# Performance work log

Hardware: AMD Instinct MI355X
Metric: run time of the kernel (lower is better)

The kernel has to match this reference:

```python
import jax, jax.numpy as jnp
import numpy as np
from jax import lax

V, D, L, H, MAXLEN = 32000, 512, 6, 8, 1024
DH = D // H
DFF = 4 * D
B, T = 8, 1024


def _ln(x, g, b, eps=1e-5):
    m = jnp.mean(x, axis=-1, keepdims=True)
    v = jnp.var(x, axis=-1, keepdims=True)
    return (x - m) * lax.rsqrt(v + eps) * g + b


def setup_inputs() -> dict:
    key = jax.random.key(0)
    ks = jax.random.split(key, 16)
    s = 0.02
    inp = {
        "idx": jax.random.randint(ks[0], (B, T), 0, V, dtype=jnp.int32),
        "wte": jax.random.normal(ks[1], (V, D), jnp.float32) * s,   # tied with head
        "wpe": jax.random.normal(ks[2], (MAXLEN, D), jnp.float32) * s,
        # per-layer stacked params [L, ...]
        "ln1_g": jnp.ones((L, D), jnp.float32),
        "ln1_b": jnp.zeros((L, D), jnp.float32),
        "w_qkv": jax.random.normal(ks[3], (L, D, 3 * D), jnp.float32) * s,
        "b_qkv": jnp.zeros((L, 3 * D), jnp.float32),
        "w_ao": jax.random.normal(ks[4], (L, D, D), jnp.float32) * s,
        "b_ao": jnp.zeros((L, D), jnp.float32),
        "ln2_g": jnp.ones((L, D), jnp.float32),
        "ln2_b": jnp.zeros((L, D), jnp.float32),
        "w_fc": jax.random.normal(ks[5], (L, D, DFF), jnp.float32) * s,
        "b_fc": jnp.zeros((L, DFF), jnp.float32),
        "w_pr": jax.random.normal(ks[6], (L, DFF, D), jnp.float32) * s,
        "b_pr": jnp.zeros((L, D), jnp.float32),
        "lnf_g": jnp.ones((D,), jnp.float32),
        "lnf_b": jnp.zeros((D,), jnp.float32),
    }
    return inp


def reference(idx, wte, wpe, ln1_g, ln1_b, w_qkv, b_qkv, w_ao, b_ao,
              ln2_g, ln2_b, w_fc, b_fc, w_pr, b_pr, lnf_g, lnf_b):
    Bx, Tx = idx.shape
    x = wte[idx] + wpe[:Tx]                      # [B,T,D]
    causal = jnp.tril(jnp.ones((Tx, Tx), bool))  # [T,T]
    scale = 1.0 / np.sqrt(DH)

    def block(x, p):
        (g1, b1, wqkv, bqkv, wao, bao, g2, b2, wfc, bfc, wpr, bpr) = p
        h = _ln(x, g1, b1)
        qkv = h @ wqkv + bqkv                    # [B,T,3D]
        q, k, v = jnp.split(qkv, 3, axis=-1)
        q = q.reshape(Bx, Tx, H, DH)
        k = k.reshape(Bx, Tx, H, DH)
        v = v.reshape(Bx, Tx, H, DH)
        att = jnp.einsum('bqhd,bkhd->bhqk', q, k) * scale
        att = jnp.where(causal, att, -jnp.inf)
        att = jax.nn.softmax(att, axis=-1)
        y = jnp.einsum('bhqk,bkhd->bqhd', att, v).reshape(Bx, Tx, D)
        x = x + y @ wao + bao
        h = _ln(x, g2, b2)
        h = jax.nn.gelu(h @ wfc + bfc, approximate=False)
        x = x + h @ wpr + bpr
        return x, None

    params = (ln1_g, ln1_b, w_qkv, b_qkv, w_ao, b_ao,
              ln2_g, ln2_b, w_fc, b_fc, w_pr, b_pr)
    x, _ = lax.scan(block, x, params)
    x = _ln(x, lnf_g, lnf_b)
    logits = x @ wte.T                           # tied head, [B,T,V]
    return logits
```

## Files before the change

### kernel.cpp

```cpp
#include <hip/hip_runtime.h>
#include <hip/hip_bf16.h>
#include <math.h>

#define V_   32000
#define D_   512
#define L_   6
#define H_   8
#define DH_  64
#define DFF_ 2048
#define B_   8
#define T_   1024
#define BT_  (B_*T_)

typedef __attribute__((ext_vector_type(4))) float f32x4;
typedef __attribute__((ext_vector_type(8))) short short8;
using bf16_t = __hip_bfloat16;

__device__ __forceinline__ float b2f(unsigned short u) {
    union { unsigned int i; float f; } v; v.i = ((unsigned int)u) << 16; return v.f;
}
__device__ __forceinline__ unsigned short f2b(float f) {
    bf16_t h = __float2bfloat16(f);
    return *reinterpret_cast<unsigned short*>(&h);
}
__device__ __forceinline__ void gl16(const void* g, void* l) {
    __builtin_amdgcn_global_load_lds((const __attribute__((address_space(1))) void*)g,
                                     (__attribute__((address_space(3))) void*)l, 16, 0, 0);
}
__device__ __forceinline__ float gelu_exact(float v) {
    return 0.5f * v * (1.0f + erff(v * 0.70710678118654752f));
}

__global__ __launch_bounds__(128) void embed_kernel(
        const int* __restrict__ idx, const float* __restrict__ wte,
        const float* __restrict__ wpe, float* __restrict__ x) {
    int bt = blockIdx.x;
    int t  = bt & (T_ - 1);
    int tok = idx[bt];
    const float4* wr = (const float4*)(wte + (size_t)tok * D_);
    const float4* pr = (const float4*)(wpe + (size_t)t * D_);
    float4* xr = (float4*)(x + (size_t)bt * D_);
    int i = threadIdx.x;
    float4 a = wr[i], b = pr[i];
    xr[i] = make_float4(a.x + b.x, a.y + b.y, a.z + b.z, a.w + b.w);
}

__global__ __launch_bounds__(128) void ln_kernel(
        const float* __restrict__ x, const float* __restrict__ g,
        const float* __restrict__ b, bf16_t* __restrict__ out) {
    int bt = blockIdx.x;
    int i  = threadIdx.x;
    float4 v = ((const float4*)(x + (size_t)bt * D_))[i];
    float s  = v.x + v.y + v.z + v.w;
    float sq = v.x*v.x + v.y*v.y + v.z*v.z + v.w*v.w;
    #pragma unroll
    for (int o = 32; o > 0; o >>= 1) {
        s  += __shfl_down(s,  o);
        sq += __shfl_down(sq, o);
    }
    __shared__ float ss[2], ssq[2];
    if ((i & 63) == 0) { ss[i >> 6] = s; ssq[i >> 6] = sq; }
    __syncthreads();
    float mean = (ss[0] + ss[1]) * (1.0f / D_);
    float var  = (ssq[0] + ssq[1]) * (1.0f / D_) - mean * mean;
    float rstd = rsqrtf(var + 1e-5f);
    float4 gg = ((const float4*)g)[i];
    float4 bb = ((const float4*)b)[i];
    ushort4 o4;
    o4.x = f2b((v.x - mean) * rstd * gg.x + bb.x);
    o4.y = f2b((v.y - mean) * rstd * gg.y + bb.y);
    o4.z = f2b((v.z - mean) * rstd * gg.z + bb.z);
    o4.w = f2b((v.w - mean) * rstd * gg.w + bb.w);
    ((ushort4*)(out + (size_t)bt * D_))[i] = o4;
}

__global__ __launch_bounds__(256) void conv_kernel(
        const float* __restrict__ s, bf16_t* __restrict__ d, int n4) {
    int i = blockIdx.x * 256 + threadIdx.x;
    if (i >= n4) return;
    float4 f = ((const float4*)s)[i];
    ushort4 u = make_ushort4(f2b(f.x), f2b(f.y), f2b(f.z), f2b(f.w));
    ((ushort4*)d)[i] = u;
}

__global__ __launch_bounds__(256) void tconv_kernel(
        const float* __restrict__ src, bf16_t* __restrict__ dst, int K, int N) {
    size_t ls = (size_t)K * N;
    const float* s = src + blockIdx.z * ls;
    bf16_t* d = dst + blockIdx.z * ls;
    __shared__ float tile[32][33];
    int n0 = blockIdx.x * 32, k0 = blockIdx.y * 32;
    int c = threadIdx.x & 31, r8 = threadIdx.x >> 5;
    #pragma unroll
    for (int i = 0; i < 4; ++i) {
        int r = r8 + i * 8;
        tile[r][c] = s[(size_t)(k0 + r) * N + n0 + c];
    }
    __syncthreads();
    #pragma unroll
    for (int i = 0; i < 4; ++i) {
        int r = r8 + i * 8;
        d[(size_t)(n0 + r) * K + k0 + c] = __float2bfloat16(tile[c][r]);
    }
}

template<int ACT, bool OBF, bool RES, bool CONVB>
__global__ __launch_bounds__(256) void mm_kernel(
        const bf16_t* __restrict__ A,
        const bf16_t* __restrict__ Bt,
        const float*  __restrict__ Bf,
        const float*  __restrict__ bias,
        const float*  __restrict__ res,
        void* __restrict__ Cout,
        int M, int N, int K)
{
    __shared__ __align__(16) unsigned short As[128 * 64];
    __shared__ __align__(16) unsigned short Bs[128 * 64];
    const int nwg = gridDim.x;
    const int orig = blockIdx.x;
    const int q8 = nwg >> 3, r8 = nwg & 7;
    const int xcd = orig & 7, lin = orig >> 3;
    const int wg = (xcd < r8) ? xcd * (q8 + 1) + lin
                              : r8 * (q8 + 1) + (xcd - r8) * q8 + lin;
    const int gym = M >> 7;
    const int by = wg % gym;
    const int bx = wg / gym;

    const int t    = threadIdx.x;
    const int row0 = by * 128;
    const int col0 = bx * 128;
    const int lane = t & 63;
    const int wid  = t >> 6;
    const int wm   = (wid & 1) * 64;
    const int wn   = (wid >> 1) * 64;
    const int fr   = lane & 15;
    const int fq   = lane >> 4;

    f32x4 acc[4][4];
    #pragma unroll
    for (int m = 0; m < 4; ++m)
        #pragma unroll
        for (int n = 0; n < 4; ++n)
            acc[m][n] = (f32x4)(0.0f);

    const unsigned short* Ab  = (const unsigned short*)A;
    const unsigned short* Btb = (const unsigned short*)Bt;

    for (int k0 = 0; k0 < K; k0 += 64) {
        __syncthreads();
        #pragma unroll
        for (int i = 0; i < 4; ++i) {
            int c = t + i * 256;
            int row = c >> 3;
            int sl  = (c & 7) ^ (row & 7);
            gl16(Ab + (size_t)(row0 + row) * K + k0 + sl * 8, As + (size_t)c * 8);
        }
        if (!CONVB) {
            #pragma unroll
            for (int i = 0; i < 4; ++i) {
                int c = t + i * 256;
                int row = c >> 3;
                int sl  = (c & 7) ^ (row & 7);
                gl16(Btb + (size_t)(col0 + row) * K + k0 + sl * 8, Bs + (size_t)c * 8);
            }
        } else {
            #pragma unroll
            for (int i = 0; i < 4; ++i) {
                int c = t + i * 256;
                int row = c >> 3;
                int sl  = (c & 7) ^ (row & 7);
                const float* sp = Bf + (size_t)(col0 + row) * K + k0 + sl * 8;
                float4 f0 = ((const float4*)sp)[0];
                float4 f1 = ((const float4*)sp)[1];
                short8 pk;
                pk[0] = f2b(f0.x); pk[1] = f2b(f0.y); pk[2] = f2b(f0.z); pk[3] = f2b(f0.w);
                pk[4] = f2b(f1.x); pk[5] = f2b(f1.y); pk[6] = f2b(f1.z); pk[7] = f2b(f1.w);
                *(short8*)(Bs + (size_t)c * 8) = pk;
            }
        }
        __syncthreads();

        #pragma unroll
        for (int kk = 0; kk < 2; ++kk) {
            short8 av[4], bv[4];
            #pragma unroll
            for (int m = 0; m < 4; ++m) {
                int R = wm + m * 16 + fr;
                int sl = (kk * 4 + fq) ^ (fr & 7);
                av[m] = *(const short8*)(As + (size_t)R * 64 + sl * 8);
            }
            #pragma unroll
            for (int n = 0; n < 4; ++n) {
                int R = wn + n * 16 + fr;
                int sl = (kk * 4 + fq) ^ (fr & 7);
                bv[n] = *(const short8*)(Bs + (size_t)R * 64 + sl * 8);
            }
            #pragma unroll
            for (int m = 0; m < 4; ++m)
                #pragma unroll
                for (int n = 0; n < 4; ++n)
                    acc[m][n] = __builtin_amdgcn_mfma_f32_16x16x32_bf16(av[m], bv[n], acc[m][n], 0, 0, 0);
        }
    }

    #pragma unroll
    for (int n = 0; n < 4; ++n) {
        int col = col0 + wn + n * 16 + fr;
        float bb = bias ? bias[col] : 0.0f;
        #pragma unroll
        for (int m = 0; m < 4; ++m) {
            int rbase = row0 + wm + m * 16 + fq * 4;
            #pragma unroll
            for (int r = 0; r < 4; ++r) {
                float v = acc[m][n][r] + bb;
                if (ACT == 1) v = gelu_exact(v);
                size_t off = (size_t)(rbase + r) * N + col;
                if (RES) v += res[off];
                if (OBF) ((bf16_t*)Cout)[off] = __float2bfloat16(v);
                else     ((float*)Cout)[off]  = v;
            }
        }
    }
}

#define MM8_PHASE(MH, NH, HALF, SRCB, R0, DSTB)                               \
  {                                                                           \
    short8 af[2][4]; short8 bg[2][2];                                         \
    _Pragma("unroll")                                                         \
    for (int ks = 0; ks < 2; ++ks) {                                          \
      _Pragma("unroll")                                                       \
      for (int m = 0; m < 4; ++m) {                                           \
        int row = ((MH)*4 + m)*32 + wm*16 + fr;                               \
        int sl  = (ks*4 + fq) ^ (fr & 7);                                     \
        af[ks][m] = *(const short8*)(curA + (size_t)row*64 + (size_t)sl*8);   \
      }                                                                       \
      _Pragma("unroll")                                                       \
      for (int n = 0; n < 2; ++n) {                                           \
        int col = ((NH)*2 + n)*64 + wn*16 + fr;                               \
        int sl  = (ks*4 + fq) ^ (fr & 7);                                     \
        bg[ks][n] = *(const short8*)(curB + (size_t)col*64 + (size_t)sl*8);   \
      }                                                                       \
    }                                                                         \
    if (pf) {                                                                 \
      _Pragma("unroll")                                                       \
      for (int i = 0; i < 2; ++i) {                                           \
        int c = (HALF)*1024 + i*512 + t;                                      \
        int row = c >> 3, sl = (c & 7) ^ (row & 7);                           \
        gl16(SRCB + (size_t)((R0) + row)*K + k0n + sl*8,                      \
             DSTB + (size_t)c*8);                                             \
      }                                                                       \
      asm volatile("s_waitcnt vmcnt(2)" ::: "memory");                        \
    } else if ((MH) == 0 && (NH) == 0) {                                      \
      asm volatile("s_waitcnt vmcnt(0)" ::: "memory");                        \
    }                                                                         \
    asm volatile("s_barrier" ::: "memory");                                   \
    asm volatile("s_waitcnt lgkmcnt(0)" ::: "memory");                        \
    __builtin_amdgcn_sched_barrier(0);                                        \
    __builtin_amdgcn_s_setprio(1);                                            \
    _Pragma("unroll")                                                         \
    for (int ks = 0; ks < 2; ++ks)                                            \
      _Pragma("unroll")                                                       \
      for (int m = 0; m < 4; ++m)                                             \
        _Pragma("unroll")                                                     \
        for (int n = 0; n < 2; ++n)                                           \
          acc[(MH)*4+m][(NH)*2+n] = __builtin_amdgcn_mfma_f32_16x16x32_bf16(  \
              af[ks][m], bg[ks][n], acc[(MH)*4+m][(NH)*2+n], 0, 0, 0);        \
    __builtin_amdgcn_s_setprio(0);                                            \
    __builtin_amdgcn_sched_barrier(0);                                        \
    asm volatile("s_barrier" ::: "memory");                                   \
  }

template<int ACT, bool OBF>
__global__ __launch_bounds__(512) void mm8_kernel(
        const bf16_t* __restrict__ A,
        const bf16_t* __restrict__ Bt,
        const float*  __restrict__ bias,
        void* __restrict__ Cout,
        int M, int N, int K)
{
    __shared__ __align__(16) unsigned short sA[2][256 * 64];
    __shared__ __align__(16) unsigned short sB[2][256 * 64];

    const int nwg = gridDim.x;
    const int orig = blockIdx.x;
    const int q8 = nwg >> 3, r8 = nwg & 7;
    const int xcd = orig & 7, lin = orig >> 3;
    const int wg = (xcd < r8) ? xcd * (q8 + 1) + lin
                              : r8 * (q8 + 1) + (xcd - r8) * q8 + lin;
    const int gym = M >> 8;
    const int by = wg % gym;
    const int bx = wg / gym;
    const int row0 = by * 256;
    const int col0 = bx * 256;

    const int t    = threadIdx.x;
    const int lane = t & 63;
    const int wid  = t >> 6;
    const int wm   = wid >> 2;
    const int wn   = wid & 3;
    const int fr   = lane & 15;
    const int fq   = lane >> 4;

    const unsigned short* Ab = (const unsigned short*)A;
    const unsigned short* Bb = (const unsigned short*)Bt;

    f32x4 acc[8][4];
    #pragma unroll
    for (int m = 0; m < 8; ++m)
        #pragma unroll
        for (int n = 0; n < 4; ++n)
            acc[m][n] = (f32x4)(0.0f);

    const int NK = K >> 6;

    #pragma unroll
    for (int h = 0; h < 2; ++h)
        #pragma unroll
        for (int i = 0; i < 2; ++i) {
            int c = h * 1024 + i * 512 + t;
            int row = c >> 3, sl = (c & 7) ^ (row & 7);
            gl16(Ab + (size_t)(row0 + row) * K + sl * 8, &sA[0][(size_t)c * 8]);
            gl16(Bb + (size_t)(col0 + row) * K + sl * 8, &sB[0][(size_t)c * 8]);
        }
    asm volatile("s_waitcnt vmcnt(0)" ::: "memory");
    asm volatile("s_barrier" ::: "memory");

    for (int s = 0; s < NK; ++s) {
        const unsigned short* curA = sA[s & 1];
        const unsigned short* curB = sB[s & 1];
        unsigned short* nxA = (unsigned short*)sA[(s + 1) & 1];
        unsigned short* nxB = (unsigned short*)sB[(s + 1) & 1];
        const int k0n = (s + 1) << 6;
        const bool pf = (s + 1) < NK;
        MM8_PHASE(0, 0, 0, Ab, row0, nxA)
        MM8_PHASE(1, 0, 0, Bb, col0, nxB)
        MM8_PHASE(0, 1, 1, Ab, row0, nxA)
        MM8_PHASE(1, 1, 1, Bb, col0, nxB)
    }

    #pragma unroll
    for (int n = 0; n < 4; ++n) {
        int col = col0 + n * 64 + wn * 16 + fr;
        float bb = bias ? bias[col] : 0.0f;
        #pragma unroll
        for (int m = 0; m < 8; ++m) {
            int rbase = row0 + m * 32 + wm * 16 + fq * 4;
            #pragma unroll
            for (int r = 0; r < 4; ++r) {
                float v = acc[m][n][r] + bb;
                if (ACT == 1) v = gelu_exact(v);
                size_t off = (size_t)(rbase + r) * N + col;
                if (OBF) ((bf16_t*)Cout)[off] = __float2bfloat16(v);
                else     ((float*)Cout)[off]  = v;
            }
        }
    }
}

__global__ __launch_bounds__(512, 2) void flash_kernel(
        const bf16_t* __restrict__ qkv, bf16_t* __restrict__ y)
{
    __shared__ __align__(16) unsigned short Ks[64][72];
    __shared__ __align__(16) unsigned short Vt[64][72];
    __shared__ __align__(16) unsigned short Pls[128][72];

    const int qt = (T_ / 128 - 1) - (blockIdx.x >> 6);
    const int bh = blockIdx.x & 63;
    const int h  = bh & (H_ - 1);
    const int b  = bh >> 3;
    const int t  = threadIdx.x;
    const int lane = t & 63;
    const int w    = t >> 6;
    const int fr   = lane & 15;
    const int fq   = lane >> 4;

    const unsigned short* qkvb = (const unsigned short*)qkv;

    short8 avq[2];
    {
        const unsigned short* qrow = qkvb +
            (size_t)(b * T_ + qt * 128 + w * 16 + fr) * (3 * D_) + h * DH_;
        avq[0] = *(const short8*)(qrow + fq * 8);
        avq[1] = *(const short8*)(qrow + 32 + fq * 8);
    }

    float mi[4], li[4];
    f32x4 oacc[4];
    #pragma unroll
    for (int r = 0; r < 4; ++r) { mi[r] = -INFINITY; li[r] = 0.0f; }
    #pragma unroll
    for (int d = 0; d < 4; ++d) oacc[d] = (f32x4)(0.0f);

    const int nt = 2 * qt + 2;
    for (int jt = 0; jt < nt; ++jt) {
        __syncthreads();
        {
            int j = t >> 3, seg = t & 7;
            const unsigned short* kr = qkvb +
                (size_t)(b * T_ + jt * 64 + j) * (3 * D_) + D_ + h * DH_ + seg * 8;
            *(short8*)&Ks[j][seg * 8] = *(const short8*)kr;
            short8 vv = *(const short8*)(kr + D_);
            int dbase = seg * 8;
            Vt[dbase + 0][j] = vv[0]; Vt[dbase + 1][j] = vv[1];
            Vt[dbase + 2][j] = vv[2]; Vt[dbase + 3][j] = vv[3];
            Vt[dbase + 4][j] = vv[4]; Vt[dbase + 5][j] = vv[5];
            Vt[dbase + 6][j] = vv[6]; Vt[dbase + 7][j] = vv[7];
        }
        __syncthreads();

        f32x4 s[4];
        #pragma unroll
        for (int jb = 0; jb < 4; ++jb) s[jb] = (f32x4)(0.0f);
        #pragma unroll
        for (int ks = 0; ks < 2; ++ks) {
            #pragma unroll
            for (int jb = 0; jb < 4; ++jb) {
                short8 bv = *(const short8*)(&Ks[jb * 16 + fr][ks * 32 + fq * 8]);
                s[jb] = __builtin_amdgcn_mfma_f32_16x16x32_bf16(avq[ks], bv, s[jb], 0, 0, 0);
            }
        }

        float sv[4][4];
        const int qgb = qt * 128 + w * 16 + fq * 4;
        #pragma unroll
        for (int jb = 0; jb < 4; ++jb) {
            int jg = jt * 64 + jb * 16 + fr;
            #pragma unroll
            for (int r = 0; r < 4; ++r) {
                float x = s[jb][r] * 0.125f;
                sv[jb][r] = (jg > qgb + r) ? -INFINITY : x;
            }
        }

        #pragma unroll
        for (int r = 0; r < 4; ++r) {
            float tm = fmaxf(fmaxf(sv[0][r], sv[1][r]), fmaxf(sv[2][r], sv[3][r]));
            tm = fmaxf(tm, __shfl_xor(tm, 1));
            tm = fmaxf(tm, __shfl_xor(tm, 2));
            tm = fmaxf(tm, __shfl_xor(tm, 4));
            tm = fmaxf(tm, __shfl_xor(tm, 8));
            float mnew = fmaxf(mi[r], tm);
            float corr = __expf(mi[r] - mnew);
            float tsum = 0.0f;
            #pragma unroll
            for (int jb = 0; jb < 4; ++jb) {
                float p = __expf(sv[jb][r] - mnew);
                sv[jb][r] = p;
                tsum += p;
            }
            tsum += __shfl_xor(tsum, 1);
            tsum += __shfl_xor(tsum, 2);
            tsum += __shfl_xor(tsum, 4);
            tsum += __shfl_xor(tsum, 8);
            li[r] = li[r] * corr + tsum;
            mi[r] = mnew;
            #pragma unroll
            for (int db = 0; db < 4; ++db) oacc[db][r] *= corr;
        }

        #pragma unroll
        for (int jb = 0; jb < 4; ++jb)
            #pragma unroll
            for (int r = 0; r < 4; ++r)
                Pls[w * 16 + fq * 4 + r][jb * 16 + fr] = f2b(sv[jb][r]);

        #pragma unroll
        for (int ks = 0; ks < 2; ++ks) {
            short8 ap = *(const short8*)(&Pls[w * 16 + fr][ks * 32 + fq * 8]);
            #pragma unroll
            for (int db = 0; db < 4; ++db) {
                short8 bv = *(const short8*)(&Vt[db * 16 + fr][ks * 32 + fq * 8]);
                oacc[db] = __builtin_amdgcn_mfma_f32_16x16x32_bf16(ap, bv, oacc[db], 0, 0, 0);
            }
        }
    }

    unsigned short* yb = (unsigned short*)y;
    #pragma unroll
    for (int r = 0; r < 4; ++r) {
        float inv = 1.0f / li[r];
        size_t row = (size_t)(b * T_ + qt * 128 + w * 16 + fq * 4 + r);
        #pragma unroll
        for (int db = 0; db < 4; ++db)
            yb[row * D_ + h * DH_ + db * 16 + fr] = f2b(oacc[db][r] * inv);
    }
}

extern "C" void kernel_launch(void* const* d_in, const int* in_sizes, int n_in,
                              void* d_out, int out_size, void* d_ws, size_t ws_size,
                              hipStream_t stream) {
    const int*   idx   = (const int*)  d_in[0];
    const float* wte   = (const float*)d_in[1];
    const float* wpe   = (const float*)d_in[2];
    const float* ln1_g = (const float*)d_in[3];
    const float* ln1_b = (const float*)d_in[4];
    const float* w_qkv = (const float*)d_in[5];
    const float* b_qkv = (const float*)d_in[6];
    const float* w_ao  = (const float*)d_in[7];
    const float* b_ao  = (const float*)d_in[8];
    const float* ln2_g = (const float*)d_in[9];
    const float* ln2_b = (const float*)d_in[10];
    const float* w_fc  = (const float*)d_in[11];
    const float* b_fc  = (const float*)d_in[12];
    const float* w_pr  = (const float*)d_in[13];
    const float* b_pr  = (const float*)d_in[14];
    const float* lnf_g = (const float*)d_in[15];
    const float* lnf_b = (const float*)d_in[16];
    float* outf = (float*)d_out;

    char* base = (char*)d_out;
    size_t off = 0;
    auto alloc = [&](size_t bytes) {
        void* p = base + off;
        off += (bytes + 255) & ~(size_t)255;
        return p;
    };
    bf16_t* wqkvT = (bf16_t*)alloc((size_t)L_ * 3 * D_ * D_ * 2);
    bf16_t* waoT  = (bf16_t*)alloc((size_t)L_ * D_ * D_ * 2);
    bf16_t* wfcT  = (bf16_t*)alloc((size_t)L_ * DFF_ * D_ * 2);
    bf16_t* wprT  = (bf16_t*)alloc((size_t)L_ * D_ * DFF_ * 2);
    bf16_t* qkvb  = (bf16_t*)alloc((size_t)BT_ * 3 * D_ * 2);
    bf16_t* yb    = (bf16_t*)alloc((size_t)BT_ * D_ * 2);
    bf16_t* hab   = (bf16_t*)alloc((size_t)BT_ * D_ * 2);
    bf16_t* fcb   = (bf16_t*)alloc((size_t)BT_ * DFF_ * 2);
    float*  xb    = (float*) alloc((size_t)BT_ * D_ * 4);

    bf16_t* hfin = (bf16_t*)d_ws;
    size_t hbytes = ((size_t)BT_ * D_ * 2 + 255) & ~(size_t)255;
    bool wte_ws = ws_size >= hbytes + (size_t)V_ * D_ * 2 + 256;
    bf16_t* wteb = wte_ws ? (bf16_t*)((char*)d_ws + hbytes) : nullptr;

    if (wte_ws)
        conv_kernel<<<(V_ * D_ / 4 + 255) / 256, 256, 0, stream>>>(wte, wteb, V_ * D_ / 4);
    tconv_kernel<<<dim3(3 * D_ / 32, D_ / 32, L_), 256, 0, stream>>>(w_qkv, wqkvT, D_, 3 * D_);
    tconv_kernel<<<dim3(D_ / 32, D_ / 32, L_), 256, 0, stream>>>(w_ao, waoT, D_, D_);
    tconv_kernel<<<dim3(DFF_ / 32, D_ / 32, L_), 256, 0, stream>>>(w_fc, wfcT, D_, DFF_);
    tconv_kernel<<<dim3(D_ / 32, DFF_ / 32, L_), 256, 0, stream>>>(w_pr, wprT, DFF_, D_);

    embed_kernel<<<BT_, 128, 0, stream>>>(idx, wte, wpe, xb);

    for (int l = 0; l < L_; ++l) {
        ln_kernel<<<BT_, 128, 0, stream>>>(xb, ln1_g + (size_t)l * D_, ln1_b + (size_t)l * D_, hab);
        mm8_kernel<0, true><<<(BT_ / 256) * (3 * D_ / 256), 512, 0, stream>>>(
            hab, wqkvT + (size_t)l * 3 * D_ * D_, b_qkv + (size_t)l * 3 * D_,
            qkvb, BT_, 3 * D_, D_);
        flash_kernel<<<512, 512, 0, stream>>>(qkvb, yb);
        mm_kernel<0, false, true, false><<<4 * 64, 256, 0, stream>>>(
            yb, waoT + (size_t)l * D_ * D_, nullptr, b_ao + (size_t)l * D_,
            xb, xb, BT_, D_, D_);
        ln_kernel<<<BT_, 128, 0, stream>>>(xb, ln2_g + (size_t)l * D_, ln2_b + (size_t)l * D_, hab);
        mm8_kernel<1, true><<<(BT_ / 256) * (DFF_ / 256), 512, 0, stream>>>(
            hab, wfcT + (size_t)l * DFF_ * D_, b_fc + (size_t)l * DFF_,
            fcb, BT_, DFF_, D_);
        mm_kernel<0, false, true, false><<<4 * 64, 256, 0, stream>>>(
            fcb, wprT + (size_t)l * D_ * DFF_, nullptr, b_pr + (size_t)l * D_,
            xb, xb, BT_, D_, DFF_);
    }

    ln_kernel<<<BT_, 128, 0, stream>>>(xb, lnf_g, lnf_b, hfin);
    if (wte_ws)
        mm8_kernel<0, false><<<(BT_ / 256) * (V_ / 256), 512, 0, stream>>>(
            hfin, wteb, nullptr, outf, BT_, V_, D_);
    else
        mm_kernel<0, false, false, true><<<250 * 64, 256, 0, stream>>>(
            hfin, nullptr, wte, nullptr, nullptr, outf, BT_, V_, D_);
}
```

Measured before the change: 1.724 ms.

## Double-buffer K/V in flash attention, widen mm K-tile, fuse embed with LN

```diff
diff --git a/kernel.cpp b/kernel.cpp
--- a/kernel.cpp
+++ b/kernel.cpp
@@ -31,18 +31,41 @@
     return 0.5f * v * (1.0f + erff(v * 0.70710678118654752f));
 }
 
-__global__ __launch_bounds__(128) void embed_kernel(
+__global__ __launch_bounds__(128) void embed_ln_kernel(
         const int* __restrict__ idx, const float* __restrict__ wte,
-        const float* __restrict__ wpe, float* __restrict__ x) {
+        const float* __restrict__ wpe, const float* __restrict__ g,
+        const float* __restrict__ bb, float* __restrict__ x,
+        bf16_t* __restrict__ hout) {
     int bt = blockIdx.x;
-    int t  = bt & (T_ - 1);
+    int tt = bt & (T_ - 1);
     int tok = idx[bt];
-    const float4* wr = (const float4*)(wte + (size_t)tok * D_);
-    const float4* pr = (const float4*)(wpe + (size_t)t * D_);
-    float4* xr = (float4*)(x + (size_t)bt * D_);
     int i = threadIdx.x;
-    float4 a = wr[i], b = pr[i];
-    xr[i] = make_float4(a.x + b.x, a.y + b.y, a.z + b.z, a.w + b.w);
+    float4 a = ((const float4*)(wte + (size_t)tok * D_))[i];
+    float4 p = ((const float4*)(wpe + (size_t)tt * D_))[i];
+    float4 v = make_float4(a.x + p.x, a.y + p.y, a.z + p.z, a.w + p.w);
+    ((float4*)(x + (size_t)bt * D_))[i] = v;
+
+    float s  = v.x + v.y + v.z + v.w;
+    float sq = v.x*v.x + v.y*v.y + v.z*v.z + v.w*v.w;
+    #pragma unroll
+    for (int o = 32; o > 0; o >>= 1) {
+        s  += __shfl_down(s,  o);
+        sq += __shfl_down(sq, o);
+    }
+    __shared__ float ss[2], ssq[2];
+    if ((i & 63) == 0) { ss[i >> 6] = s; ssq[i >> 6] = sq; }
+    __syncthreads();
+    float mean = (ss[0] + ss[1]) * (1.0f / D_);
+    float var  = (ssq[0] + ssq[1]) * (1.0f / D_) - mean * mean;
+    float rstd = rsqrtf(var + 1e-5f);
+    float4 gg = ((const float4*)g)[i];
+    float4 b2 = ((const float4*)bb)[i];
+    ushort4 o4;
+    o4.x = f2b((v.x - mean) * rstd * gg.x + b2.x);
+    o4.y = f2b((v.y - mean) * rstd * gg.y + b2.y);
+    o4.z = f2b((v.z - mean) * rstd * gg.z + b2.z);
+    o4.w = f2b((v.w - mean) * rstd * gg.w + b2.w);
+    ((ushort4*)(hout + (size_t)bt * D_))[i] = o4;
 }
 
 __global__ __launch_bounds__(128) void ln_kernel(
@@ -104,7 +127,7 @@
     }
 }
 
-template<int ACT, bool OBF, bool RES, bool CONVB>
+template<int BK, int ACT, bool OBF, bool RES, bool CONVB>
 __global__ __launch_bounds__(256) void mm_kernel(
         const bf16_t* __restrict__ A,
         const bf16_t* __restrict__ Bt,
@@ -114,8 +137,10 @@
         void* __restrict__ Cout,
         int M, int N, int K)
 {
-    __shared__ __align__(16) unsigned short As[128 * 64];
-    __shared__ __align__(16) unsigned short Bs[128 * 64];
+    constexpr int SLOTS = BK / 8;
+    constexpr int CH    = BK / 16;
+    __shared__ __align__(16) unsigned short As[128 * BK];
+    __shared__ __align__(16) unsigned short Bs[128 * BK];
     const int nwg = gridDim.x;
     const int orig = blockIdx.x;
     const int q8 = nwg >> 3, r8 = nwg & 7;
@@ -146,29 +171,29 @@
     const unsigned short* Ab  = (const unsigned short*)A;
     const unsigned short* Btb = (const unsigned short*)Bt;
 
-    for (int k0 = 0; k0 < K; k0 += 64) {
+    for (int k0 = 0; k0 < K; k0 += BK) {
         __syncthreads();
         #pragma unroll
-        for (int i = 0; i < 4; ++i) {
+        for (int i = 0; i < CH; ++i) {
             int c = t + i * 256;
-            int row = c >> 3;
-            int sl  = (c & 7) ^ (row & 7);
+            int row = c / SLOTS;
+            int sl  = (c & (SLOTS - 1)) ^ (row & 7);
             gl16(Ab + (size_t)(row0 + row) * K + k0 + sl * 8, As + (size_t)c * 8);
         }
         if (!CONVB) {
             #pragma unroll
-            for (int i = 0; i < 4; ++i) {
+            for (int i = 0; i < CH; ++i) {
                 int c = t + i * 256;
-                int row = c >> 3;
-                int sl  = (c & 7) ^ (row & 7);
+                int row = c / SLOTS;
+                int sl  = (c & (SLOTS - 1)) ^ (row & 7);
                 gl16(Btb + (size_t)(col0 + row) * K + k0 + sl * 8, Bs + (size_t)c * 8);
             }
         } else {
             #pragma unroll
-            for (int i = 0; i < 4; ++i) {
+            for (int i = 0; i < CH; ++i) {
                 int c = t + i * 256;
-                int row = c >> 3;
-                int sl  = (c & 7) ^ (row & 7);
+                int row = c / SLOTS;
+                int sl  = (c & (SLOTS - 1)) ^ (row & 7);
                 const float* sp = Bf + (size_t)(col0 + row) * K + k0 + sl * 8;
                 float4 f0 = ((const float4*)sp)[0];
                 float4 f1 = ((const float4*)sp)[1];
@@ -181,19 +206,19 @@
         __syncthreads();
 
         #pragma unroll
-        for (int kk = 0; kk < 2; ++kk) {
+        for (int kk = 0; kk < BK / 32; ++kk) {
             short8 av[4], bv[4];
             #pragma unroll
             for (int m = 0; m < 4; ++m) {
                 int R = wm + m * 16 + fr;
                 int sl = (kk * 4 + fq) ^ (fr & 7);
-                av[m] = *(const short8*)(As + (size_t)R * 64 + sl * 8);
+                av[m] = *(const short8*)(As + (size_t)R * BK + sl * 8);
             }
             #pragma unroll
             for (int n = 0; n < 4; ++n) {
                 int R = wn + n * 16 + fr;
                 int sl = (kk * 4 + fq) ^ (fr & 7);
-                bv[n] = *(const short8*)(Bs + (size_t)R * 64 + sl * 8);
+                bv[n] = *(const short8*)(Bs + (size_t)R * BK + sl * 8);
             }
             #pragma unroll
             for (int m = 0; m < 4; ++m)
@@ -360,8 +385,8 @@
 __global__ __launch_bounds__(512, 2) void flash_kernel(
         const bf16_t* __restrict__ qkv, bf16_t* __restrict__ y)
 {
-    __shared__ __align__(16) unsigned short Ks[64][72];
-    __shared__ __align__(16) unsigned short Vt[64][72];
+    __shared__ __align__(16) unsigned short Ks[2][64][72];
+    __shared__ __align__(16) unsigned short Vt[2][64][72];
     __shared__ __align__(16) unsigned short Pls[128][72];
 
     const int qt = (T_ / 128 - 1) - (blockIdx.x >> 6);
@@ -373,6 +398,8 @@
     const int w    = t >> 6;
     const int fr   = lane & 15;
     const int fq   = lane >> 4;
+    const int sj   = t >> 3;
+    const int sseg = t & 7;
 
     const unsigned short* qkvb = (const unsigned short*)qkv;
 
@@ -392,21 +419,33 @@
     for (int d = 0; d < 4; ++d) oacc[d] = (f32x4)(0.0f);
 
     const int nt = 2 * qt + 2;
+
+    short8 kreg, vreg;
+    {
+        const unsigned short* kr = qkvb +
+            (size_t)(b * T_ + sj) * (3 * D_) + D_ + h * DH_ + sseg * 8;
+        kreg = *(const short8*)kr;
+        vreg = *(const short8*)(kr + D_);
+    }
+    *(short8*)&Ks[0][sj][sseg * 8] = kreg;
+    {
+        int dbase = sseg * 8;
+        Vt[0][dbase + 0][sj] = vreg[0]; Vt[0][dbase + 1][sj] = vreg[1];
+        Vt[0][dbase + 2][sj] = vreg[2]; Vt[0][dbase + 3][sj] = vreg[3];
+        Vt[0][dbase + 4][sj] = vreg[4]; Vt[0][dbase + 5][sj] = vreg[5];
+        Vt[0][dbase + 6][sj] = vreg[6]; Vt[0][dbase + 7][sj] = vreg[7];
+    }
+    __syncthreads();
+
     for (int jt = 0; jt < nt; ++jt) {
-        __syncthreads();
-        {
-            int j = t >> 3, seg = t & 7;
+        const int cur = jt & 1;
+        const bool pf = (jt + 1) < nt;
+        if (pf) {
             const unsigned short* kr = qkvb +
-                (size_t)(b * T_ + jt * 64 + j) * (3 * D_) + D_ + h * DH_ + seg * 8;
-            *(short8*)&Ks[j][seg * 8] = *(const short8*)kr;
-            short8 vv = *(const short8*)(kr + D_);
-            int dbase = seg * 8;
-            Vt[dbase + 0][j] = vv[0]; Vt[dbase + 1][j] = vv[1];
-            Vt[dbase + 2][j] = vv[2]; Vt[dbase + 3][j] = vv[3];
-            Vt[dbase + 4][j] = vv[4]; Vt[dbase + 5][j] = vv[5];
-            Vt[dbase + 6][j] = vv[6]; Vt[dbase + 7][j] = vv[7];
-        }
-        __syncthreads();
+                (size_t)(b * T_ + (jt + 1) * 64 + sj) * (3 * D_) + D_ + h * DH_ + sseg * 8;
+            kreg = *(const short8*)kr;
+            vreg = *(const short8*)(kr + D_);
+        }
 
         f32x4 s[4];
         #pragma unroll
@@ -415,7 +454,7 @@
         for (int ks = 0; ks < 2; ++ks) {
             #pragma unroll
             for (int jb = 0; jb < 4; ++jb) {
-                short8 bv = *(const short8*)(&Ks[jb * 16 + fr][ks * 32 + fq * 8]);
+                short8 bv = *(const short8*)(&Ks[cur][jb * 16 + fr][ks * 32 + fq * 8]);
                 s[jb] = __builtin_amdgcn_mfma_f32_16x16x32_bf16(avq[ks], bv, s[jb], 0, 0, 0);
             }
         }
@@ -469,10 +508,21 @@
             short8 ap = *(const short8*)(&Pls[w * 16 + fr][ks * 32 + fq * 8]);
             #pragma unroll
             for (int db = 0; db < 4; ++db) {
-                short8 bv = *(const short8*)(&Vt[db * 16 + fr][ks * 32 + fq * 8]);
+                short8 bv = *(const short8*)(&Vt[cur][db * 16 + fr][ks * 32 + fq * 8]);
                 oacc[db] = __builtin_amdgcn_mfma_f32_16x16x32_bf16(ap, bv, oacc[db], 0, 0, 0);
             }
         }
+
+        __syncthreads();
+        if (pf) {
+            *(short8*)&Ks[cur ^ 1][sj][sseg * 8] = kreg;
+            int dbase = sseg * 8;
+            Vt[cur ^ 1][dbase + 0][sj] = vreg[0]; Vt[cur ^ 1][dbase + 1][sj] = vreg[1];
+            Vt[cur ^ 1][dbase + 2][sj] = vreg[2]; Vt[cur ^ 1][dbase + 3][sj] = vreg[3];
+            Vt[cur ^ 1][dbase + 4][sj] = vreg[4]; Vt[cur ^ 1][dbase + 5][sj] = vreg[5];
+            Vt[cur ^ 1][dbase + 6][sj] = vreg[6]; Vt[cur ^ 1][dbase + 7][sj] = vreg[7];
+        }
+        __syncthreads();
     }
 
     unsigned short* yb = (unsigned short*)y;
@@ -537,31 +587,34 @@
     tconv_kernel<<<dim3(DFF_ / 32, D_ / 32, L_), 256, 0, stream>>>(w_fc, wfcT, D_, DFF_);
     tconv_kernel<<<dim3(D_ / 32, DFF_ / 32, L_), 256, 0, stream>>>(w_pr, wprT, DFF_, D_);
 
-    embed_kernel<<<BT_, 128, 0, stream>>>(idx, wte, wpe, xb);
+    embed_ln_kernel<<<BT_, 128, 0, stream>>>(idx, wte, wpe, ln1_g, ln1_b, xb, hab);
 
     for (int l = 0; l < L_; ++l) {
-        ln_kernel<<<BT_, 128, 0, stream>>>(xb, ln1_g + (size_t)l * D_, ln1_b + (size_t)l * D_, hab);
         mm8_kernel<0, true><<<(BT_ / 256) * (3 * D_ / 256), 512, 0, stream>>>(
             hab, wqkvT + (size_t)l * 3 * D_ * D_, b_qkv + (size_t)l * 3 * D_,
             qkvb, BT_, 3 * D_, D_);
         flash_kernel<<<512, 512, 0, stream>>>(qkvb, yb);
-        mm_kernel<0, false, true, false><<<4 * 64, 256, 0, stream>>>(
+        mm_kernel<128, 0, false, true, false><<<4 * 64, 256, 0, stream>>>(
             yb, waoT + (size_t)l * D_ * D_, nullptr, b_ao + (size_t)l * D_,
             xb, xb, BT_, D_, D_);
         ln_kernel<<<BT_, 128, 0, stream>>>(xb, ln2_g + (size_t)l * D_, ln2_b + (size_t)l * D_, hab);
         mm8_kernel<1, true><<<(BT_ / 256) * (DFF_ / 256), 512, 0, stream>>>(
             hab, wfcT + (size_t)l * DFF_ * D_, b_fc + (size_t)l * DFF_,
             fcb, BT_, DFF_, D_);
-        mm_kernel<0, false, true, false><<<4 * 64, 256, 0, stream>>>(
+        mm_kernel<128, 0, false, true, false><<<4 * 64, 256, 0, stream>>>(
             fcb, wprT + (size_t)l * D_ * DFF_, nullptr, b_pr + (size_t)l * D_,
             xb, xb, BT_, D_, DFF_);
-    }
-
-    ln_kernel<<<BT_, 128, 0, stream>>>(xb, lnf_g, lnf_b, hfin);
+        if (l < L_ - 1)
+            ln_kernel<<<BT_, 128, 0, stream>>>(xb, ln1_g + (size_t)(l + 1) * D_,
+                                               ln1_b + (size_t)(l + 1) * D_, hab);
+        else
+            ln_kernel<<<BT_, 128, 0, stream>>>(xb, lnf_g, lnf_b, hfin);
+    }
+
     if (wte_ws)
         mm8_kernel<0, false><<<(BT_ / 256) * (V_ / 256), 512, 0, stream>>>(
             hfin, wteb, nullptr, outf, BT_, V_, D_);
     else
-        mm_kernel<0, false, false, true><<<250 * 64, 256, 0, stream>>>(
+        mm_kernel<64, 0, false, false, true><<<250 * 64, 256, 0, stream>>>(
             hfin, nullptr, wte, nullptr, nullptr, outf, BT_, V_, D_);
 }
```

After: 1.688 ms. 1.02x faster.
